# Optimization experiments

Measured on AMD Instinct MI355X. Metric: run time of the kernel, lower is better.

The kernel has to match this reference:

```python
import jax, jax.numpy as jnp
import numpy as np

B, V, CIN, H, W = 2, 4, 256, 96, 96
COUT, VS = 32, 64


def setup_inputs() -> dict:
    key = jax.random.key(0)
    k1, k2, k3, k4, k5 = jax.random.split(key, 5)
    features = jax.random.normal(k1, (B, V, CIN, H, W), dtype=jnp.float32)
    proj_matricies = jax.random.normal(k2, (B, V, 3, 4), dtype=jnp.float32)
    coord_volumes = jax.random.normal(k3, (B, VS, VS, VS, 3), dtype=jnp.float32) * 1000.0
    W_proc = jax.random.normal(k4, (COUT, CIN), dtype=jnp.float32) * 0.05
    b_proc = jax.random.normal(k5, (COUT,), dtype=jnp.float32) * 0.01
    return {"features": features, "proj_matricies": proj_matricies,
            "coord_volumes": coord_volumes, "W_proc": W_proc, "b_proc": b_proc}


def _bilinear_sample(feat, x, y):
    # feat: [C, H, W]; x, y: [N] pixel coords (align_corners=True mapping already applied)
    Hh, Ww = feat.shape[1], feat.shape[2]
    x0 = jnp.floor(x).astype(jnp.int32); x1 = x0 + 1
    y0 = jnp.floor(y).astype(jnp.int32); y1 = y0 + 1
    wx1 = x - x0; wx0 = 1.0 - wx1
    wy1 = y - y0; wy0 = 1.0 - wy1

    def gather(xi, yi):
        valid = ((xi >= 0) & (xi < Ww) & (yi >= 0) & (yi < Hh)).astype(feat.dtype)
        xc = jnp.clip(xi, 0, Ww - 1); yc = jnp.clip(yi, 0, Hh - 1)
        return feat[:, yc, xc] * valid  # [C, N] (zeros padding)

    return (gather(x0, y0) * (wx0 * wy0)
            + gather(x1, y0) * (wx1 * wy0)
            + gather(x0, y1) * (wx0 * wy1)
            + gather(x1, y1) * (wx1 * wy1))


def reference(features, proj_matricies, coord_volumes, W_proc, b_proc):
    b, v, cin, h, w = features.shape
    vs = coord_volumes.shape[1]
    # 1x1 conv (process_feature)
    feats = jnp.einsum('bvchw,oc->bvohw', features, W_proc) + b_proc[None, None, :, None, None]
    c = feats.shape[2]
    # homogeneous 3D grid points: [B, N, 4]
    pts = coord_volumes.reshape(b, -1, 3)
    pts_h = jnp.concatenate([pts, jnp.ones(pts.shape[:-1] + (1,), pts.dtype)], axis=-1)
    # project to image plane: [B, V, N, 3] homogeneous (u, v, w)
    proj_pts = jnp.einsum('bvij,bnj->bvni', proj_matricies, pts_h)
    wz = proj_pts[..., 2]
    invalid = wz <= 0.0
    wz_safe = jnp.where(wz == 0.0, 1.0, wz)
    u = proj_pts[..., 0] / wz_safe
    ve = proj_pts[..., 1] / wz_safe
    # normalized grid coords (faithful to original: x divided by feature_shape[0]=H, y by feature_shape[1]=W)
    gx = 2.0 * (u / h - 0.5)
    gy = 2.0 * (ve / w - 0.5)
    # align_corners=True pixel coords: x indexes width, y indexes height
    px = (gx + 1.0) * 0.5 * (w - 1)
    py = (gy + 1.0) * 0.5 * (h - 1)
    # sample per (batch, view): [B, V, C, N]
    sampled = jax.vmap(jax.vmap(_bilinear_sample))(feats, px, py)
    sampled = jnp.where(invalid[:, :, None, :], 0.0, sampled)
    # softmax over views per (b, c, voxel), weighted sum
    weights = jax.nn.softmax(sampled, axis=1)
    vol = jnp.sum(sampled * weights, axis=1)  # [B, C, N]
    return vol.reshape(b, c, vs, vs, vs)
```

## Files before the change

kernel.cpp:

```cpp
#include <hip/hip_runtime.h>
#include <hip/hip_bf16.h>

#define CIN   256
#define COUT  32
#define IMG_H 96
#define IMG_W 96
#define HW    (IMG_H*IMG_W)
#define NB    2
#define NV    4
#define VSZ   64
#define NVOX  (VSZ*VSZ*VSZ)

__global__ __launch_bounds__(256) void conv1x1_kernel(
    const float* __restrict__ features,
    const float* __restrict__ Wp,
    const float* __restrict__ bp,
    __hip_bfloat16* __restrict__ out)
{
    const int og   = __builtin_amdgcn_readfirstlane((threadIdx.x >> 6) & 3);
    const int lane = threadIdx.x & 63;
    const int bv   = blockIdx.y;
    const int px   = blockIdx.x*64 + lane;
    const float* f     = features + (size_t)bv*CIN*HW + px;
    const float* wbase = Wp + (size_t)og*8*CIN;

    float acc[8];
    #pragma unroll
    for (int j = 0; j < 8; ++j) acc[j] = bp[og*8 + j];

    for (int cc = 0; cc < CIN; cc += 8) {
        float x[8];
        #pragma unroll
        for (int i = 0; i < 8; ++i)
            x[i] = f[(size_t)(cc + i)*HW];
        #pragma unroll
        for (int i = 0; i < 8; ++i) {
            #pragma unroll
            for (int j = 0; j < 8; ++j)
                acc[j] += x[i] * wbase[(size_t)j*CIN + cc + i];
        }
    }

    union { uint4 u4; __hip_bfloat16 h[8]; } pk;
    #pragma unroll
    for (int j = 0; j < 8; ++j) pk.h[j] = __float2bfloat16(acc[j]);
    *(uint4*)(out + ((size_t)(bv*HW + px))*COUT + og*8) = pk.u4;
}

__global__ __launch_bounds__(256) void volgen_kernel(
    const __hip_bfloat16* __restrict__ feats,
    const float* __restrict__ proj,
    const float* __restrict__ coords,
    float* __restrict__ out)
{
    __shared__ float T[COUT*65];
    const int tid = threadIdx.x;
    const int vl  = tid >> 2;
    const int cg  = tid & 3;
    const int b   = blockIdx.y;
    const int n   = blockIdx.x*64 + vl;

    const float* cp = coords + ((size_t)b*NVOX + n)*3;
    const float X = cp[0], Y = cp[1], Z = cp[2];

    int   off[NV][4];
    float wgt[NV][4];
    #pragma unroll
    for (int v = 0; v < NV; ++v) {
        const float* P = proj + (size_t)(b*NV + v)*12;
        const float wz = P[8]*X + P[9]*Y + P[10]*Z + P[11];
        const bool  vz = wz > 0.f;
        const float rz = __builtin_amdgcn_rcpf(wz);
        float px = (P[0]*X + P[1]*Y + P[2]*Z + P[3]) * rz * (95.f/96.f);
        float py = (P[4]*X + P[5]*Y + P[6]*Z + P[7]) * rz * (95.f/96.f);
        px = vz ? px : 0.f;  py = vz ? py : 0.f;
        px = fminf(fmaxf(px, -1.0e6f), 1.0e6f);
        py = fminf(fmaxf(py, -1.0e6f), 1.0e6f);
        const float fx0 = floorf(px), fy0 = floorf(py);
        const int x0 = (int)fx0, y0 = (int)fy0, x1 = x0+1, y1 = y0+1;
        const float wx1 = px - fx0, wx0 = 1.f - wx1;
        const float wy1 = py - fy0, wy0 = 1.f - wy1;
        const bool vx0 = (unsigned)x0 < (unsigned)IMG_W;
        const bool vx1 = (unsigned)x1 < (unsigned)IMG_W;
        const bool vy0 = (unsigned)y0 < (unsigned)IMG_H;
        const bool vy1 = (unsigned)y1 < (unsigned)IMG_H;
        const int cx0 = min(max(x0, 0), IMG_W-1), cx1 = min(max(x1, 0), IMG_W-1);
        const int cy0 = min(max(y0, 0), IMG_H-1), cy1 = min(max(y1, 0), IMG_H-1);
        const int base = ((b*NV + v)*HW)*COUT + cg*8;
        off[v][0] = base + (cy0*IMG_W + cx0)*COUT;  wgt[v][0] = (vz & vx0 & vy0) ? wx0*wy0 : 0.f;
        off[v][1] = base + (cy0*IMG_W + cx1)*COUT;  wgt[v][1] = (vz & vx1 & vy0) ? wx1*wy0 : 0.f;
        off[v][2] = base + (cy1*IMG_W + cx0)*COUT;  wgt[v][2] = (vz & vx0 & vy1) ? wx0*wy1 : 0.f;
        off[v][3] = base + (cy1*IMG_W + cx1)*COUT;  wgt[v][3] = (vz & vx1 & vy1) ? wx1*wy1 : 0.f;
    }

    uint4 t[NV][4];
    #pragma unroll
    for (int v = 0; v < NV; ++v)
        #pragma unroll
        for (int c = 0; c < 4; ++c)
            t[v][c] = *(const uint4*)(feats + off[v][c]);

    float A[8], Bs[8];
    #pragma unroll
    for (int j = 0; j < 8; ++j) { A[j] = 0.f; Bs[j] = 0.f; }

    #pragma unroll
    for (int v = 0; v < NV; ++v) {
        float s[8];
        #pragma unroll
        for (int j = 0; j < 8; ++j) s[j] = 0.f;
        #pragma unroll
        for (int c = 0; c < 4; ++c) {
            const float w = wgt[v][c];
            const unsigned tu[4] = { t[v][c].x, t[v][c].y, t[v][c].z, t[v][c].w };
            #pragma unroll
            for (int k = 0; k < 4; ++k) {
                s[2*k]   += w * __uint_as_float(tu[k] << 16);
                s[2*k+1] += w * __uint_as_float(tu[k] & 0xffff0000u);
            }
        }
        #pragma unroll
        for (int j = 0; j < 8; ++j) {
            const float e = __expf(s[j]);
            A[j] += e;  Bs[j] += s[j]*e;
        }
    }

    #pragma unroll
    for (int j = 0; j < 8; ++j)
        T[(cg*8 + j)*65 + vl] = Bs[j] * __builtin_amdgcn_rcpf(A[j]);
    __syncthreads();

    const size_t ob = (size_t)b*COUT*NVOX + (size_t)blockIdx.x*64;
    #pragma unroll
    for (int i = 0; i < 8; ++i) {
        const int idx = i*256 + tid;
        const int ch = idx >> 6, vx = idx & 63;
        out[ob + (size_t)ch*NVOX + vx] = T[ch*65 + vx];
    }
}

extern "C" void kernel_launch(void* const* d_in, const int* in_sizes, int n_in,
                              void* d_out, int out_size, void* d_ws, size_t ws_size,
                              hipStream_t stream)
{
    const float* features = (const float*)d_in[0];
    const float* proj     = (const float*)d_in[1];
    const float* coords   = (const float*)d_in[2];
    const float* Wp       = (const float*)d_in[3];
    const float* bp       = (const float*)d_in[4];
    float* out = (float*)d_out;
    __hip_bfloat16* featsT = (__hip_bfloat16*)d_ws;

    hipLaunchKernelGGL(conv1x1_kernel, dim3(HW/64, NB*NV), dim3(256), 0, stream,
                       features, Wp, bp, featsT);
    hipLaunchKernelGGL(volgen_kernel, dim3(NVOX/64, NB), dim3(256), 0, stream,
                       featsT, proj, coords, out);
}
```

Measured before the change: 189.2 us.

## Map one voxel per thread in volgen and drop shared-memory transpose

The volume kernel now gives each thread one voxel across all 32 channels in chunks of 8, instead of splitting channels over 4 threads per voxel. Projection math is no longer repeated four times per voxel, output stores go straight to global memory coalesced across voxels, and the LDS transpose and barrier are gone. Packed float2 vector types are used in the hope of emitting packed FMA instructions. In exchange, each thread issues four times as many gathers and holds more live registers, and the grid shrinks by 4x, which may reduce occupancy and latency hiding for the random gathers.

Measured after the change: 179.9 us. 1.05x faster.

```diff
diff --git a/kernel.cpp b/kernel.cpp
--- a/kernel.cpp
+++ b/kernel.cpp
@@ -10,6 +10,8 @@
 #define NV    4
 #define VSZ   64
 #define NVOX  (VSZ*VSZ*VSZ)
+
+typedef __attribute__((ext_vector_type(2))) float f32x2;
 
 __global__ __launch_bounds__(256) void conv1x1_kernel(
     const float* __restrict__ features,
@@ -53,12 +55,9 @@
     const float* __restrict__ coords,
     float* __restrict__ out)
 {
-    __shared__ float T[COUT*65];
     const int tid = threadIdx.x;
-    const int vl  = tid >> 2;
-    const int cg  = tid & 3;
     const int b   = blockIdx.y;
-    const int n   = blockIdx.x*64 + vl;
+    const int n   = blockIdx.x*256 + tid;
 
     const float* cp = coords + ((size_t)b*NVOX + n)*3;
     const float X = cp[0], Y = cp[1], Z = cp[2];
@@ -86,57 +85,59 @@
         const bool vy1 = (unsigned)y1 < (unsigned)IMG_H;
         const int cx0 = min(max(x0, 0), IMG_W-1), cx1 = min(max(x1, 0), IMG_W-1);
         const int cy0 = min(max(y0, 0), IMG_H-1), cy1 = min(max(y1, 0), IMG_H-1);
-        const int base = ((b*NV + v)*HW)*COUT + cg*8;
+        const int base = ((b*NV + v)*HW)*COUT;
         off[v][0] = base + (cy0*IMG_W + cx0)*COUT;  wgt[v][0] = (vz & vx0 & vy0) ? wx0*wy0 : 0.f;
         off[v][1] = base + (cy0*IMG_W + cx1)*COUT;  wgt[v][1] = (vz & vx1 & vy0) ? wx1*wy0 : 0.f;
         off[v][2] = base + (cy1*IMG_W + cx0)*COUT;  wgt[v][2] = (vz & vx0 & vy1) ? wx0*wy1 : 0.f;
         off[v][3] = base + (cy1*IMG_W + cx1)*COUT;  wgt[v][3] = (vz & vx1 & vy1) ? wx1*wy1 : 0.f;
     }
 
-    uint4 t[NV][4];
-    #pragma unroll
-    for (int v = 0; v < NV; ++v)
-        #pragma unroll
-        for (int c = 0; c < 4; ++c)
-            t[v][c] = *(const uint4*)(feats + off[v][c]);
-
-    float A[8], Bs[8];
-    #pragma unroll
-    for (int j = 0; j < 8; ++j) { A[j] = 0.f; Bs[j] = 0.f; }
+    const size_t ob = (size_t)b*COUT*NVOX + n;
 
     #pragma unroll
-    for (int v = 0; v < NV; ++v) {
-        float s[8];
+    for (int ch0 = 0; ch0 < COUT; ch0 += 8) {
+        f32x2 A2[4], B2[4];
         #pragma unroll
-        for (int j = 0; j < 8; ++j) s[j] = 0.f;
+        for (int k = 0; k < 4; ++k) { A2[k] = (f32x2)(0.f); B2[k] = (f32x2)(0.f); }
+
         #pragma unroll
-        for (int c = 0; c < 4; ++c) {
-            const float w = wgt[v][c];
-            const unsigned tu[4] = { t[v][c].x, t[v][c].y, t[v][c].z, t[v][c].w };
+        for (int v = 0; v < NV; ++v) {
+            uint4 t[4];
+            #pragma unroll
+            for (int c = 0; c < 4; ++c)
+                t[c] = *(const uint4*)(feats + off[v][c] + ch0);
+
+            f32x2 s2[4];
+            #pragma unroll
+            for (int k = 0; k < 4; ++k) s2[k] = (f32x2)(0.f);
+
+            #pragma unroll
+            for (int c = 0; c < 4; ++c) {
+                const f32x2 w2 = (f32x2)(wgt[v][c]);
+                const unsigned tu[4] = { t[c].x, t[c].y, t[c].z, t[c].w };
+                #pragma unroll
+                for (int k = 0; k < 4; ++k) {
+                    f32x2 f2;
+                    f2.x = __uint_as_float(tu[k] << 16);
+                    f2.y = __uint_as_float(tu[k] & 0xffff0000u);
+                    s2[k] += w2 * f2;
+                }
+            }
             #pragma unroll
             for (int k = 0; k < 4; ++k) {
-                s[2*k]   += w * __uint_as_float(tu[k] << 16);
-                s[2*k+1] += w * __uint_as_float(tu[k] & 0xffff0000u);
+                f32x2 e2;
+                e2.x = __expf(s2[k].x);
+                e2.y = __expf(s2[k].y);
+                A2[k] += e2;
+                B2[k] += s2[k]*e2;
             }
         }
+
         #pragma unroll
-        for (int j = 0; j < 8; ++j) {
-            const float e = __expf(s[j]);
-            A[j] += e;  Bs[j] += s[j]*e;
+        for (int k = 0; k < 4; ++k) {
+            out[ob + (size_t)(ch0 + 2*k    )*NVOX] = B2[k].x * __builtin_amdgcn_rcpf(A2[k].x);
+            out[ob + (size_t)(ch0 + 2*k + 1)*NVOX] = B2[k].y * __builtin_amdgcn_rcpf(A2[k].y);
         }
-    }
-
-    #pragma unroll
-    for (int j = 0; j < 8; ++j)
-        T[(cg*8 + j)*65 + vl] = Bs[j] * __builtin_amdgcn_rcpf(A[j]);
-    __syncthreads();
-
-    const size_t ob = (size_t)b*COUT*NVOX + (size_t)blockIdx.x*64;
-    #pragma unroll
-    for (int i = 0; i < 8; ++i) {
-        const int idx = i*256 + tid;
-        const int ch = idx >> 6, vx = idx & 63;
-        out[ob + (size_t)ch*NVOX + vx] = T[ch*65 + vx];
     }
 }
 
@@ -154,6 +155,6 @@
 
     hipLaunchKernelGGL(conv1x1_kernel, dim3(HW/64, NB*NV), dim3(256), 0, stream,
                        features, Wp, bp, featsT);
-    hipLaunchKernelGGL(volgen_kernel, dim3(NVOX/64, NB), dim3(256), 0, stream,
+    hipLaunchKernelGGL(volgen_kernel, dim3(NVOX/256, NB), dim3(256), 0, stream,
                        featsT, proj, coords, out);
 }
```
